# Kernel optimization log

Hardware: AMD Instinct MI355X
Metric: run time of the kernel (lower is better)

The kernel has to match this reference:

```python
import jax, jax.numpy as jnp
import numpy as np

IN_C = 128
MID_C = 128
EPS = 1e-5


def layer_norm(x, g, b):
    mu = jnp.mean(x, axis=-1, keepdims=True)
    var = jnp.mean(jnp.square(x - mu), axis=-1, keepdims=True)
    return (x - mu) * jax.lax.rsqrt(var + EPS) * g + b


def setup_inputs() -> dict:
    key = jax.random.key(0)
    ks = jax.random.split(key, 16)
    B, N = 1, 384
    s_in = 1.0 / np.sqrt(IN_C)
    s_mid = 1.0 / np.sqrt(MID_C)
    return {
        "x2d": jax.random.normal(ks[0], (B, N, N, IN_C), dtype=jnp.float32),
        "n1_g": jnp.ones((IN_C,), jnp.float32),
        "n1_b": jnp.zeros((IN_C,), jnp.float32),
        "n2_g": jnp.ones((MID_C,), jnp.float32),
        "n2_b": jnp.zeros((MID_C,), jnp.float32),
        "w1i": jax.random.uniform(ks[1], (MID_C, IN_C), jnp.float32, -s_in, s_in),
        "b1i": jnp.zeros((MID_C,), jnp.float32),
        "w1j": jax.random.uniform(ks[2], (MID_C, IN_C), jnp.float32, -s_in, s_in),
        "b1j": jnp.zeros((MID_C,), jnp.float32),
        "w1i_s": jax.random.uniform(ks[3], (MID_C, IN_C), jnp.float32, -s_in, s_in),
        "b1i_s": jnp.zeros((MID_C,), jnp.float32),
        "w1j_s": jax.random.uniform(ks[4], (MID_C, IN_C), jnp.float32, -s_in, s_in),
        "b1j_s": jnp.zeros((MID_C,), jnp.float32),
        "w2": jax.random.uniform(ks[5], (IN_C, MID_C), jnp.float32, -s_mid, s_mid),
        "b2": jnp.zeros((IN_C,), jnp.float32),
        "w3": jax.random.uniform(ks[6], (IN_C, IN_C), jnp.float32, -s_in, s_in),
        "b3": jnp.zeros((IN_C,), jnp.float32),
    }


def reference(x2d, n1_g, n1_b, n2_g, n2_b, w1i, b1i, w1j, b1j,
              w1i_s, b1i_s, w1j_s, b1j_s, w2, b2, w3, b3):
    # x2d: [B, N, N, C]
    x = layer_norm(x2d, n1_g, n1_b)
    i = (x @ w1i.T + b1i) * jax.nn.sigmoid(x @ w1i_s.T + b1i_s)  # [B,N,N,mid]
    j = (x @ w1j.T + b1j) * jax.nn.sigmoid(x @ w1j_s.T + b1j_s)  # [B,N,N,mid]
    out = jnp.einsum('bikc,bjkc->bijc', i, j)                    # contract over k
    out = layer_norm(out, n2_g, n2_b)
    out = out @ w2.T + b2
    out = out * jax.nn.sigmoid(x @ w3.T + b3)
    return out
```

## Files before the change

### kernel.cpp

```cpp
#include <hip/hip_runtime.h>

#define NN 384
#define CC 128
#define NPOS (NN * NN)

typedef short bf8_t __attribute__((ext_vector_type(8)));
typedef float f32x4_t __attribute__((ext_vector_type(4)));

#define MFMA16(a, b, c) __builtin_amdgcn_mfma_f32_16x16x32_bf16((a), (b), (c), 0, 0, 0)

__device__ __forceinline__ unsigned short f2bf(float f) {
  unsigned int u = __builtin_bit_cast(unsigned int, f);
  u += 0x7fffu + ((u >> 16) & 1u);
  return (unsigned short)(u >> 16);
}
__device__ __forceinline__ float bf2f(unsigned short s) {
  return __builtin_bit_cast(float, ((unsigned int)s) << 16);
}
__device__ __forceinline__ float sigm(float x) { return 1.0f / (1.0f + __expf(-x)); }

__global__ __launch_bounds__(256) void kW(const float* __restrict__ a,
                                          const float* __restrict__ b,
                                          const float* __restrict__ c,
                                          const float* __restrict__ d,
                                          const float* __restrict__ e,
                                          const float* __restrict__ f,
                                          unsigned short* __restrict__ o) {
  int idx = (blockIdx.x * 256 + threadIdx.x) * 4;
  const float* s = f;
  if (idx < 16384) s = a;
  else if (idx < 32768) s = b;
  else if (idx < 49152) s = c;
  else if (idx < 65536) s = d;
  else if (idx < 81920) s = e;
  int off = idx & 16383;
  float4 v = *(const float4*)(s + off);
  o[idx + 0] = f2bf(v.x);
  o[idx + 1] = f2bf(v.y);
  o[idx + 2] = f2bf(v.z);
  o[idx + 3] = f2bf(v.w);
}

__global__ __launch_bounds__(256) void kLN(const float* __restrict__ x,
                                           const float* __restrict__ n1g,
                                           const float* __restrict__ n1b,
                                           unsigned short* __restrict__ x_ln) {
  int t = threadIdx.x;
  int pos = blockIdx.x * 128 + (t >> 1);
  int half = t & 1;
  const float* xr = x + (size_t)pos * CC + half * 64;
  float v[64];
  float s = 0.f;
#pragma unroll
  for (int a = 0; a < 16; ++a) {
    float4 f4 = ((const float4*)xr)[a];
    v[4 * a + 0] = f4.x; v[4 * a + 1] = f4.y;
    v[4 * a + 2] = f4.z; v[4 * a + 3] = f4.w;
    s += f4.x + f4.y + f4.z + f4.w;
  }
  s += __shfl_xor(s, 1);
  float mu = s * (1.0f / CC);
  float vs = 0.f;
#pragma unroll
  for (int a = 0; a < 64; ++a) { float d = v[a] - mu; vs += d * d; }
  vs += __shfl_xor(vs, 1);
  float rs = rsqrtf(vs * (1.0f / CC) + 1e-5f);
  unsigned short* dst = x_ln + (size_t)pos * CC + half * 64;
#pragma unroll
  for (int a8 = 0; a8 < 8; ++a8) {
    union { bf8_t v8; unsigned short e[8]; } u;
#pragma unroll
    for (int e = 0; e < 8; ++e) {
      int c = half * 64 + a8 * 8 + e;
      u.e[e] = f2bf((v[a8 * 8 + e] - mu) * rs * n1g[c] + n1b[c]);
    }
    *(bf8_t*)(dst + a8 * 8) = u.v8;
  }
}

__global__ __launch_bounds__(256, 2) void kP(
    const unsigned short* __restrict__ x_ln, const unsigned short* __restrict__ wcat,
    const float* __restrict__ b1i, const float* __restrict__ b1is,
    const float* __restrict__ b1j, const float* __restrict__ b1js,
    const float* __restrict__ b3v, unsigned short* __restrict__ i_s,
    unsigned short* __restrict__ j_s, unsigned short* __restrict__ g3) {
  __shared__ __align__(16) unsigned short lds[16640];
  float* bl = (float*)(lds + 16384);

  int b = blockIdx.x;
  int pt = b / 6, job = b % 6;
  int p = job >> 1, h = job & 1;
  int p0 = pt * 128;
  int t = threadIdx.x, lane = t & 63, wave = t >> 6;
  int lr = lane & 15, lh = lane >> 4;

  bf8_t xf[2][4];
#pragma unroll
  for (int nt = 0; nt < 2; ++nt)
#pragma unroll
    for (int kk = 0; kk < 4; ++kk)
      xf[nt][kk] = *(const bf8_t*)(x_ln + (size_t)(p0 + wave * 32 + nt * 16 + lr) * CC +
                                   kk * 32 + lh * 8);

  int mV = p * 2;
  const unsigned short* Wv = wcat + (size_t)mV * CC * CC + h * 64 * CC;
#pragma unroll
  for (int it = 0; it < 4; ++it) {
    int u = it * 256 + t;
    int row = u >> 4, sl = u & 15;
    int slg = sl ^ (row & 7);
    __builtin_amdgcn_global_load_lds(
        (const __attribute__((address_space(1))) unsigned int*)(Wv + row * CC + slg * 8),
        (__attribute__((address_space(3))) unsigned int*)(lds + u * 8), 16, 0, 0);
  }
  if (p < 2) {
    const unsigned short* Wg = wcat + (size_t)(mV + 1) * CC * CC + h * 64 * CC;
#pragma unroll
    for (int it = 0; it < 4; ++it) {
      int u = it * 256 + t;
      int row = u >> 4, sl = u & 15;
      int slg = sl ^ (row & 7);
      __builtin_amdgcn_global_load_lds(
          (const __attribute__((address_space(1))) unsigned int*)(Wg + row * CC + slg * 8),
          (__attribute__((address_space(3))) unsigned int*)(lds + 8192 + u * 8), 16, 0, 0);
    }
  }
  {
    const float* bvp = (p == 0) ? b1i : (p == 1) ? b1j : b3v;
    if (t < 16) ((float4*)bl)[t] = ((const float4*)(bvp + h * 64))[t];
    if (p < 2 && t >= 16 && t < 32) {
      const float* bgp = (p == 0) ? b1is : b1js;
      ((float4*)bl)[t] = ((const float4*)(bgp + h * 64))[t - 16];
    }
  }
  __syncthreads();

  f32x4_t z4 = {0.f, 0.f, 0.f, 0.f};
  f32x4_t accV[2][4], accG[2][4];
#pragma unroll
  for (int nt = 0; nt < 2; ++nt)
#pragma unroll
    for (int ct = 0; ct < 4; ++ct) { accV[nt][ct] = z4; accG[nt][ct] = z4; }
#pragma unroll
  for (int ct = 0; ct < 4; ++ct)
#pragma unroll
    for (int kk = 0; kk < 4; ++kk) {
      int rv = ct * 16 + lr;
      int slot = (kk * 4 + lh) ^ (rv & 7);
      bf8_t wv = *(const bf8_t*)&lds[rv * 128 + slot * 8];
      if (p < 2) {
        bf8_t wg = *(const bf8_t*)&lds[8192 + rv * 128 + slot * 8];
#pragma unroll
        for (int nt = 0; nt < 2; ++nt) {
          accV[nt][ct] = MFMA16(wv, xf[nt][kk], accV[nt][ct]);
          accG[nt][ct] = MFMA16(wg, xf[nt][kk], accG[nt][ct]);
        }
      } else {
#pragma unroll
        for (int nt = 0; nt < 2; ++nt)
          accV[nt][ct] = MFMA16(xf[nt][kk], wv, accV[nt][ct]);
      }
    }
  __syncthreads();

  if (p < 2) {
#pragma unroll
    for (int nt = 0; nt < 2; ++nt)
#pragma unroll
      for (int ct = 0; ct < 4; ++ct)
#pragma unroll
        for (int r = 0; r < 4; ++r) {
          int cl = ct * 16 + lh * 4 + r;
          int pos = wave * 32 + nt * 16 + lr;
          float o = (accV[nt][ct][r] + bl[cl]) * sigm(accG[nt][ct][r] + bl[64 + cl]);
          int sw = ((ct * 4 + lh) & 7) << 4;
          lds[cl * 128 + (pos ^ sw)] = f2bf(o);
        }
    __syncthreads();
    unsigned short* dstm = p ? j_s : i_s;
#pragma unroll
    for (int it = 0; it < 4; ++it) {
      int u = it * 256 + t;
      int cl = u >> 4, ch = u & 15;
      int s = (cl >> 2) & 7;
      bf8_t v = *(const bf8_t*)&lds[cl * 128 + ((ch ^ (s << 1)) * 8)];
      *(bf8_t*)(dstm + (size_t)(h * 64 + cl) * NPOS + p0 + ch * 8) = v;
    }
  } else {
#pragma unroll
    for (int nt = 0; nt < 2; ++nt)
#pragma unroll
      for (int ct = 0; ct < 4; ++ct)
#pragma unroll
        for (int r = 0; r < 4; ++r) {
          int pos = wave * 32 + nt * 16 + lh * 4 + r;
          int cl = ct * 16 + lr;
          float o = sigm(accV[nt][ct][r] + bl[cl]);
          int slot = (cl >> 3) ^ (pos & 7);
          lds[pos * 64 + slot * 8 + (cl & 7)] = f2bf(o);
        }
    __syncthreads();
#pragma unroll
    for (int it = 0; it < 4; ++it) {
      int u = it * 256 + t;
      int pos = u >> 3, ch = u & 7;
      int slot = ch ^ (pos & 7);
      bf8_t v = *(const bf8_t*)&lds[pos * 64 + slot * 8];
      *(bf8_t*)(g3 + (size_t)(p0 + pos) * CC + h * 64 + ch * 8) = v;
    }
  }
}

__global__ __launch_bounds__(256) void kB(const unsigned short* __restrict__ i_s,
                                          const unsigned short* __restrict__ j_s,
                                          float* __restrict__ out_pre) {
  __shared__ unsigned short At[128][32];
  __shared__ unsigned short Bt[128][32];
  int b = blockIdx.x;
  int logical = (b & 7) * 144 + (b >> 3);
  int c = logical / 9;
  int tt = logical % 9;
  int i0 = (tt / 3) * 128, j0 = (tt % 3) * 128;
  const unsigned short* Ab = i_s + ((size_t)c * NN + i0) * NN;
  const unsigned short* Bb = j_s + ((size_t)c * NN + j0) * NN;
  int t = threadIdx.x, lane = t & 63, wave = t >> 6;
  int wi = (wave >> 1) * 64, wj = (wave & 1) * 64;
  int lr = lane & 15, lh = lane >> 4;
  int rsub = lane >> 2;
  int ksub = (lane & 3) * 8;

  f32x4_t z4 = {0.f, 0.f, 0.f, 0.f};
  f32x4_t acc[4][4];
#pragma unroll
  for (int mt = 0; mt < 4; ++mt)
#pragma unroll
    for (int nt = 0; nt < 4; ++nt) acc[mt][nt] = z4;

  for (int k0 = 0; k0 < NN; k0 += 32) {
#pragma unroll
    for (int half = 0; half < 2; ++half) {
      int r = half * 64 + wave * 16;
      __builtin_amdgcn_global_load_lds(
          (const __attribute__((address_space(1))) unsigned int*)(Ab + (size_t)(r + rsub) * NN + k0 + ksub),
          (__attribute__((address_space(3))) unsigned int*)&At[r][0], 16, 0, 0);
      __builtin_amdgcn_global_load_lds(
          (const __attribute__((address_space(1))) unsigned int*)(Bb + (size_t)(r + rsub) * NN + k0 + ksub),
          (__attribute__((address_space(3))) unsigned int*)&Bt[r][0], 16, 0, 0);
    }
    __syncthreads();
    bf8_t af2[4], bf2[4];
#pragma unroll
    for (int mt = 0; mt < 4; ++mt) af2[mt] = *(const bf8_t*)&At[wi + mt * 16 + lr][lh * 8];
#pragma unroll
    for (int nt = 0; nt < 4; ++nt) bf2[nt] = *(const bf8_t*)&Bt[wj + nt * 16 + lr][lh * 8];
#pragma unroll
    for (int mt = 0; mt < 4; ++mt)
#pragma unroll
      for (int nt = 0; nt < 4; ++nt) acc[mt][nt] = MFMA16(af2[mt], bf2[nt], acc[mt][nt]);
    __syncthreads();
  }
  float* orow = out_pre + ((size_t)c * NN + (i0 + wi)) * NN + (j0 + wj);
#pragma unroll
  for (int mt = 0; mt < 4; ++mt)
#pragma unroll
    for (int nt = 0; nt < 4; ++nt)
#pragma unroll
      for (int r = 0; r < 4; ++r)
        orow[(size_t)(mt * 16 + lh * 4 + r) * NN + nt * 16 + lr] = acc[mt][nt][r];
}

__global__ __launch_bounds__(256) void kC(const float* __restrict__ out_pre,
                                          const float* __restrict__ n2g,
                                          const float* __restrict__ n2b,
                                          const unsigned short* __restrict__ w2bf,
                                          const float* __restrict__ b2,
                                          const unsigned short* __restrict__ g3,
                                          float* __restrict__ out) {
  __shared__ unsigned short xs2[128][136];
  int b = blockIdx.x;
  int ii = b / 3, j0 = (b % 3) * 128;
  int t = threadIdx.x, lane = t & 63, wave = t >> 6;
  {
    int pos = t >> 1, half = t & 1;
    const float* src = out_pre + (size_t)half * 64 * NPOS + (size_t)ii * NN + j0 + pos;
    float v[64];
    float s = 0.f;
#pragma unroll
    for (int a2 = 0; a2 < 64; ++a2) { v[a2] = src[(size_t)a2 * NPOS]; s += v[a2]; }
    s += __shfl_xor(s, 1);
    float mu = s * (1.0f / CC);
    float vs = 0.f;
#pragma unroll
    for (int a2 = 0; a2 < 64; ++a2) { float d = v[a2] - mu; vs += d * d; }
    vs += __shfl_xor(vs, 1);
    float rs = rsqrtf(vs * (1.0f / CC) + 1e-5f);
#pragma unroll
    for (int a8 = 0; a8 < 8; ++a8) {
      union { bf8_t v8; unsigned short e[8]; } u;
#pragma unroll
      for (int e2 = 0; e2 < 8; ++e2) {
        int c = half * 64 + a8 * 8 + e2;
        u.e[e2] = f2bf((v[a8 * 8 + e2] - mu) * rs * n2g[c] + n2b[c]);
      }
      *(bf8_t*)&xs2[pos][half * 64 + a8 * 8] = u.v8;
    }
  }
  __syncthreads();
  int lr = lane & 15, lh = lane >> 4;
  bf8_t af2[2][4];
#pragma unroll
  for (int mt = 0; mt < 2; ++mt)
#pragma unroll
    for (int kk = 0; kk < 4; ++kk)
      af2[mt][kk] = *(const bf8_t*)&xs2[wave * 32 + mt * 16 + lr][kk * 32 + lh * 8];
  f32x4_t z4 = {0.f, 0.f, 0.f, 0.f};
  f32x4_t acc[2][8];
#pragma unroll
  for (int mt = 0; mt < 2; ++mt)
#pragma unroll
    for (int nt = 0; nt < 8; ++nt) acc[mt][nt] = z4;
#pragma unroll
  for (int nt = 0; nt < 8; ++nt) {
#pragma unroll
    for (int kk = 0; kk < 4; ++kk) {
      bf8_t bw = *(const bf8_t*)(w2bf + (size_t)(nt * 16 + lr) * CC + kk * 32 + lh * 8);
#pragma unroll
      for (int mt = 0; mt < 2; ++mt) acc[mt][nt] = MFMA16(af2[mt][kk], bw, acc[mt][nt]);
    }
  }
#pragma unroll
  for (int mt = 0; mt < 2; ++mt)
#pragma unroll
    for (int nt = 0; nt < 8; ++nt)
#pragma unroll
      for (int r = 0; r < 4; ++r) {
        int posl = wave * 32 + mt * 16 + lh * 4 + r;
        int c = nt * 16 + lr;
        size_t p = (size_t)ii * NN + j0 + posl;
        float y = acc[mt][nt][r] + b2[c];
        out[p * CC + c] = y * bf2f(g3[p * CC + c]);
      }
}

extern "C" void kernel_launch(void* const* d_in, const int* in_sizes, int n_in,
                              void* d_out, int out_size, void* d_ws, size_t ws_size,
                              hipStream_t stream) {
  (void)in_sizes; (void)n_in; (void)out_size; (void)ws_size;
  const float* x2d  = (const float*)d_in[0];
  const float* n1g  = (const float*)d_in[1];
  const float* n1b  = (const float*)d_in[2];
  const float* n2g  = (const float*)d_in[3];
  const float* n2b  = (const float*)d_in[4];
  const float* w1i  = (const float*)d_in[5];
  const float* b1i  = (const float*)d_in[6];
  const float* w1j  = (const float*)d_in[7];
  const float* b1j  = (const float*)d_in[8];
  const float* w1is = (const float*)d_in[9];
  const float* b1is = (const float*)d_in[10];
  const float* w1js = (const float*)d_in[11];
  const float* b1js = (const float*)d_in[12];
  const float* w2   = (const float*)d_in[13];
  const float* b2   = (const float*)d_in[14];
  const float* w3   = (const float*)d_in[15];
  const float* b3   = (const float*)d_in[16];

  char* ws = (char*)d_ws;
  unsigned short* wcat = (unsigned short*)ws;
  size_t TELEMS = (size_t)CC * NN * NN;
  unsigned short* i_s  = (unsigned short*)(ws + 262144);
  unsigned short* j_s  = i_s + TELEMS;
  unsigned short* g3   = j_s + TELEMS;
  unsigned short* x_ln = g3 + TELEMS;
  float* out_pre = (float*)x_ln;
  float* outp = (float*)d_out;

  kW<<<96, 256, 0, stream>>>(w1i, w1is, w1j, w1js, w3, w2, wcat);
  kLN<<<1152, 256, 0, stream>>>(x2d, n1g, n1b, x_ln);
  kP<<<6912, 256, 0, stream>>>(x_ln, wcat, b1i, b1is, b1j, b1js, b3, i_s, j_s, g3);
  kB<<<1152, 256, 0, stream>>>(i_s, j_s, out_pre);
  kC<<<1152, 256, 0, stream>>>(out_pre, n2g, n2b, wcat + 5 * CC * CC, b2, g3, outp);
}
```

Measured before the change: 195.0 us.

## Use packed bf16 conversion, remap kP blocks per XCD, hoist bias loads

Replaces the software round-to-nearest float-to-bf16 conversion with the packed hardware v_cvt_pk_bf16_f32 instruction in the weight-cast, both layernorm kernels and the projection epilogue. It also remaps kP block indices so that consecutive position tiles land on the same XCD, aiming for better L2 locality of the shared x_ln tile across the six jobs. Bias values are hoisted from LDS into registers before the MFMA loop. The hardware conversion could round NaN or edge cases differently, and the XCD remap assumes the grid size is a multiple of 8 tiles of 144.

After: 218.0 us. +11.8%, slower.

```diff
diff --git a/kernel.cpp b/kernel.cpp
--- a/kernel.cpp
+++ b/kernel.cpp
@@ -13,6 +13,11 @@
   unsigned int u = __builtin_bit_cast(unsigned int, f);
   u += 0x7fffu + ((u >> 16) & 1u);
   return (unsigned short)(u >> 16);
+}
+__device__ __forceinline__ unsigned int f2bf2(float a, float b) {
+  unsigned int r;
+  asm("v_cvt_pk_bf16_f32 %0, %1, %2" : "=v"(r) : "v"(a), "v"(b));
+  return r;
 }
 __device__ __forceinline__ float bf2f(unsigned short s) {
   return __builtin_bit_cast(float, ((unsigned int)s) << 16);
@@ -35,10 +40,10 @@
   else if (idx < 81920) s = e;
   int off = idx & 16383;
   float4 v = *(const float4*)(s + off);
-  o[idx + 0] = f2bf(v.x);
-  o[idx + 1] = f2bf(v.y);
-  o[idx + 2] = f2bf(v.z);
-  o[idx + 3] = f2bf(v.w);
+  uint2 w;
+  w.x = f2bf2(v.x, v.y);
+  w.y = f2bf2(v.z, v.w);
+  *(uint2*)(o + idx) = w;
 }
 
 __global__ __launch_bounds__(256) void kLN(const float* __restrict__ x,
@@ -68,11 +73,13 @@
   unsigned short* dst = x_ln + (size_t)pos * CC + half * 64;
 #pragma unroll
   for (int a8 = 0; a8 < 8; ++a8) {
-    union { bf8_t v8; unsigned short e[8]; } u;
-#pragma unroll
-    for (int e = 0; e < 8; ++e) {
-      int c = half * 64 + a8 * 8 + e;
-      u.e[e] = f2bf((v[a8 * 8 + e] - mu) * rs * n1g[c] + n1b[c]);
+    union { bf8_t v8; unsigned int w[4]; } u;
+#pragma unroll
+    for (int q = 0; q < 4; ++q) {
+      int c0 = half * 64 + a8 * 8 + q * 2;
+      float y0 = (v[a8 * 8 + q * 2 + 0] - mu) * rs * n1g[c0] + n1b[c0];
+      float y1 = (v[a8 * 8 + q * 2 + 1] - mu) * rs * n1g[c0 + 1] + n1b[c0 + 1];
+      u.w[q] = f2bf2(y0, y1);
     }
     *(bf8_t*)(dst + a8 * 8) = u.v8;
   }
@@ -88,7 +95,9 @@
   float* bl = (float*)(lds + 16384);
 
   int b = blockIdx.x;
-  int pt = b / 6, job = b % 6;
+  int xcd = b & 7, m = b >> 3;
+  int tl = m / 6, job = m % 6;
+  int pt = xcd * 144 + tl;
   int p = job >> 1, h = job & 1;
   int p0 = pt * 128;
   int t = threadIdx.x, lane = t & 63, wave = t >> 6;
@@ -135,6 +144,20 @@
   }
   __syncthreads();
 
+  float blv[16], blg[16];
+  if (p < 2) {
+#pragma unroll
+    for (int ct = 0; ct < 4; ++ct)
+#pragma unroll
+      for (int r = 0; r < 4; ++r) {
+        blv[ct * 4 + r] = bl[ct * 16 + lh * 4 + r];
+        blg[ct * 4 + r] = bl[64 + ct * 16 + lh * 4 + r];
+      }
+  } else {
+#pragma unroll
+    for (int ct = 0; ct < 4; ++ct) blv[ct] = bl[ct * 16 + lr];
+  }
+
   f32x4_t z4 = {0.f, 0.f, 0.f, 0.f};
   f32x4_t accV[2][4], accG[2][4];
 #pragma unroll
@@ -167,15 +190,23 @@
 #pragma unroll
     for (int nt = 0; nt < 2; ++nt)
 #pragma unroll
-      for (int ct = 0; ct < 4; ++ct)
-#pragma unroll
-        for (int r = 0; r < 4; ++r) {
-          int cl = ct * 16 + lh * 4 + r;
-          int pos = wave * 32 + nt * 16 + lr;
-          float o = (accV[nt][ct][r] + bl[cl]) * sigm(accG[nt][ct][r] + bl[64 + cl]);
-          int sw = ((ct * 4 + lh) & 7) << 4;
-          lds[cl * 128 + (pos ^ sw)] = f2bf(o);
+      for (int ct = 0; ct < 4; ++ct) {
+        int pos = wave * 32 + nt * 16 + lr;
+        int sw = ((ct * 4 + lh) & 7) << 4;
+        int px = pos ^ sw;
+#pragma unroll
+        for (int rp = 0; rp < 2; ++rp) {
+          int r0 = rp * 2;
+          int cl = ct * 16 + lh * 4 + r0;
+          float o0 = (accV[nt][ct][r0] + blv[ct * 4 + r0]) *
+                     sigm(accG[nt][ct][r0] + blg[ct * 4 + r0]);
+          float o1 = (accV[nt][ct][r0 + 1] + blv[ct * 4 + r0 + 1]) *
+                     sigm(accG[nt][ct][r0 + 1] + blg[ct * 4 + r0 + 1]);
+          unsigned int pk = f2bf2(o0, o1);
+          lds[cl * 128 + px] = (unsigned short)pk;
+          lds[(cl + 1) * 128 + px] = (unsigned short)(pk >> 16);
         }
+      }
     __syncthreads();
     unsigned short* dstm = p ? j_s : i_s;
 #pragma unroll
@@ -190,15 +221,21 @@
 #pragma unroll
     for (int nt = 0; nt < 2; ++nt)
 #pragma unroll
-      for (int ct = 0; ct < 4; ++ct)
-#pragma unroll
-        for (int r = 0; r < 4; ++r) {
-          int pos = wave * 32 + nt * 16 + lh * 4 + r;
-          int cl = ct * 16 + lr;
-          float o = sigm(accV[nt][ct][r] + bl[cl]);
-          int slot = (cl >> 3) ^ (pos & 7);
-          lds[pos * 64 + slot * 8 + (cl & 7)] = f2bf(o);
+      for (int ct = 0; ct < 4; ++ct) {
+        int cl = ct * 16 + lr;
+#pragma unroll
+        for (int rp = 0; rp < 2; ++rp) {
+          int r0 = rp * 2;
+          int pos0 = wave * 32 + nt * 16 + lh * 4 + r0;
+          float o0 = sigm(accV[nt][ct][r0] + blv[ct]);
+          float o1 = sigm(accV[nt][ct][r0 + 1] + blv[ct]);
+          unsigned int pk = f2bf2(o0, o1);
+          int slot0 = (cl >> 3) ^ (pos0 & 7);
+          int slot1 = (cl >> 3) ^ ((pos0 + 1) & 7);
+          lds[pos0 * 64 + slot0 * 8 + (cl & 7)] = (unsigned short)pk;
+          lds[(pos0 + 1) * 64 + slot1 * 8 + (cl & 7)] = (unsigned short)(pk >> 16);
         }
+      }
     __syncthreads();
 #pragma unroll
     for (int it = 0; it < 4; ++it) {
@@ -296,11 +333,13 @@
     float rs = rsqrtf(vs * (1.0f / CC) + 1e-5f);
 #pragma unroll
     for (int a8 = 0; a8 < 8; ++a8) {
-      union { bf8_t v8; unsigned short e[8]; } u;
-#pragma unroll
-      for (int e2 = 0; e2 < 8; ++e2) {
-        int c = half * 64 + a8 * 8 + e2;
-        u.e[e2] = f2bf((v[a8 * 8 + e2] - mu) * rs * n2g[c] + n2b[c]);
+      union { bf8_t v8; unsigned int w[4]; } u;
+#pragma unroll
+      for (int q = 0; q < 4; ++q) {
+        int c0 = half * 64 + a8 * 8 + q * 2;
+        float y0 = (v[a8 * 8 + q * 2 + 0] - mu) * rs * n2g[c0] + n2b[c0];
+        float y1 = (v[a8 * 8 + q * 2 + 1] - mu) * rs * n2g[c0 + 1] + n2b[c0 + 1];
+        u.w[q] = f2bf2(y0, y1);
       }
       *(bf8_t*)&xs2[pos][half * 64 + a8 * 8] = u.v8;
     }
```
